# Kernel optimization log

Hardware: AMD Instinct MI355X
Metric: run time of the kernel (lower is better)

Reference implementation:

```python
import jax, jax.numpy as jnp
import numpy as np

B, T, C, H = 4, 2048, 2048, 16
DH = C // H  # 128

def setup_inputs() -> dict:
    key = jax.random.key(0)
    ks = jax.random.split(key, 5)
    s_in = 1.0 / np.sqrt(C)
    return {
        "x": jax.random.normal(ks[0], (B, T, C), dtype=jnp.float32),
        "qkv_w": jax.random.uniform(ks[1], (3 * C, C), jnp.float32, -s_in, s_in),
        "qkv_b": jax.random.uniform(ks[2], (3 * C,), jnp.float32, -s_in, s_in),
        "proj_w": jax.random.uniform(ks[3], (C, C), jnp.float32, -s_in, s_in),
        "proj_b": jax.random.uniform(ks[4], (C,), jnp.float32, -s_in, s_in),
    }

def reference(x, qkv_w, qkv_b, proj_w, proj_b):
    b, t, _ = x.shape
    qkv = x @ qkv_w.T + qkv_b                     # [B,T,3C]
    q, k, v = jnp.split(qkv, 3, axis=-1)
    # [B,T,C] -> [B,H,T,Dh]
    q = q.reshape(b, t, H, DH).transpose(0, 2, 1, 3)
    k = k.reshape(b, t, H, DH).transpose(0, 2, 1, 3)
    v = v.reshape(b, t, H, DH).transpose(0, 2, 1, 3)
    scores = jnp.einsum('bhqd,bhkd->bhqk', q, k) / jnp.sqrt(jnp.float32(DH))
    causal = jnp.tril(jnp.ones((t, t), dtype=bool))  # [T,T]
    scores = jnp.where(causal[None, None], scores, jnp.finfo(scores.dtype).min)
    att = jax.nn.softmax(scores, axis=-1)
    out = jnp.einsum('bhqk,bhkd->bhqd', att, v)   # [B,H,T,Dh]
    out = out.transpose(0, 2, 1, 3).reshape(b, t, C)
    return out @ proj_w.T + proj_b
```

## Files before the change

kernel.cpp:

```cpp
#include <hip/hip_runtime.h>
#include <stdint.h>


typedef __attribute__((ext_vector_type(8))) short bf8_t;
typedef __attribute__((ext_vector_type(4))) float f4_t;

__device__ __forceinline__ short f2bf(float f) {
  union { float f; uint32_t u; } x; x.f = f;
  uint32_t r = x.u + 0x7fffu + ((x.u >> 16) & 1u);
  return (short)(r >> 16);
}

#define GLD16(gp, lp) __builtin_amdgcn_global_load_lds( \
    (const __attribute__((address_space(1))) void*)(gp), \
    (__attribute__((address_space(3))) void*)(lp), 16, 0, 0)

#define QSCALE (0.08838834764831845f * 1.4426950408889634f)

__global__ __launch_bounds__(256) void cast3_f32_bf16(
    const float* __restrict__ a, const float* __restrict__ b,
    const float* __restrict__ c, short* __restrict__ oa,
    short* __restrict__ ob, short* __restrict__ oc,
    int na4, int nb4, int nc4) {
  int i = blockIdx.x * blockDim.x + threadIdx.x;
  const float* src; short* dst; int idx;
  if (i < na4) { src = a; dst = oa; idx = i; }
  else if (i < na4 + nb4) { src = b; dst = ob; idx = i - na4; }
  else if (i < na4 + nb4 + nc4) { src = c; dst = oc; idx = i - na4 - nb4; }
  else return;
  float4 v = ((const float4*)src)[idx];
  short4 o;
  o.x = f2bf(v.x); o.y = f2bf(v.y); o.z = f2bf(v.z); o.w = f2bf(v.w);
  ((short4*)dst)[idx] = o;
}

template <int MODE>
__global__ __launch_bounds__(256) void gemm_bt(
    const short* __restrict__ A, const short* __restrict__ Bw,
    const float* __restrict__ bias, float* __restrict__ Cout,
    short* __restrict__ Qo, short* __restrict__ Ko, short* __restrict__ Vo,
    int M, int N, int K) {
  __shared__ __attribute__((aligned(16))) short lA[8192];
  __shared__ __attribute__((aligned(16))) short lB[8192];
  const int tid = threadIdx.x;
  const int lane = tid & 63, wave = tid >> 6;
  const int quad = lane >> 4, l16 = lane & 15;
  const int wm = wave >> 1, wn = wave & 1;
  const int m0 = blockIdx.y * 128, n0 = blockIdx.x * 128;
  const int which = (MODE == 0) ? (n0 >> 11) : -1;
  const bool swapAB = (MODE == 0) && (which == 2);

  f4_t acc[4][4];
  if (!swapAB) {
#pragma unroll
    for (int j = 0; j < 4; ++j) {
      const float b0 = bias[n0 + wn * 64 + j * 16 + l16];
      const f4_t bv = {b0, b0, b0, b0};
#pragma unroll
      for (int i = 0; i < 4; ++i) acc[i][j] = bv;
    }
  } else {
#pragma unroll
    for (int i = 0; i < 4; ++i)
#pragma unroll
      for (int r = 0; r < 4; ++r) {
        const float b0 = bias[n0 + wn * 64 + i * 16 + quad * 4 + r];
#pragma unroll
        for (int j = 0; j < 4; ++j) acc[i][j][r] = b0;
      }
  }

  const char* baseA = (const char*)(A + (size_t)m0 * K);
  const char* baseB = (const char*)(Bw + (size_t)n0 * K);
  uint32_t voff[4];
#pragma unroll
  for (int r = 0; r < 4; ++r) {
    const int off = tid * 16 + r * 4096;
    const int kk = off >> 13;
    const int row = (off >> 6) & 127;
    const int col = kk * 32 + ((off & 63) >> 1);
    voff[r] = (uint32_t)(row * K + col) * 2u;
  }

  for (int k0 = 0; k0 < K; k0 += 64) {
    __syncthreads();
#pragma unroll
    for (int r = 0; r < 4; ++r) {
      const int off = tid * 16 + r * 4096;
      GLD16(baseA + voff[r], (char*)lA + off);
      GLD16(baseB + voff[r], (char*)lB + off);
    }
    baseA += 128;
    baseB += 128;
    __syncthreads();
#pragma unroll
    for (int kk = 0; kk < 2; ++kk) {
      bf8_t af[4], bfr[4];
#pragma unroll
      for (int i = 0; i < 4; ++i) {
        af[i]  = *(const bf8_t*)(lA + kk * 4096 + (wm * 64 + i * 16 + l16) * 32 + quad * 8);
        bfr[i] = *(const bf8_t*)(lB + kk * 4096 + (wn * 64 + i * 16 + l16) * 32 + quad * 8);
      }
      if (!swapAB) {
#pragma unroll
        for (int i = 0; i < 4; ++i)
#pragma unroll
          for (int j = 0; j < 4; ++j)
            acc[i][j] = __builtin_amdgcn_mfma_f32_16x16x32_bf16(af[i], bfr[j], acc[i][j], 0, 0, 0);
      } else {
#pragma unroll
        for (int i = 0; i < 4; ++i)
#pragma unroll
          for (int j = 0; j < 4; ++j)
            acc[i][j] = __builtin_amdgcn_mfma_f32_16x16x32_bf16(bfr[i], af[j], acc[i][j], 0, 0, 0);
      }
    }
  }

  if (MODE == 1) {
    const int mb = m0 + wm * 64, nb = n0 + wn * 64;
#pragma unroll
    for (int i = 0; i < 4; ++i) {
#pragma unroll
      for (int r = 0; r < 4; ++r) {
        const int m = mb + i * 16 + quad * 4 + r;
#pragma unroll
        for (int j = 0; j < 4; ++j) {
          const int n = nb + j * 16 + l16;
          Cout[(size_t)m * N + n] = acc[i][j][r];
        }
      }
    }
  } else if (!swapAB) {
    const int mb = m0 + wm * 64, nb = n0 + wn * 64;
    const int b = m0 >> 11;
    const int h = (n0 & 2047) >> 7;
    short* dst = (which == 0) ? Qo : Ko;
    const float sc = (which == 0) ? QSCALE : 1.0f;
#pragma unroll
    for (int i = 0; i < 4; ++i) {
#pragma unroll
      for (int r = 0; r < 4; ++r) {
        const int t = (mb + i * 16 + quad * 4 + r) & 2047;
#pragma unroll
        for (int j = 0; j < 4; ++j) {
          const int d = (nb + j * 16 + l16) & 127;
          dst[((size_t)((b * 16 + h) * 2048 + t)) * 128 + d] =
              f2bf(acc[i][j][r] * sc);
        }
      }
    }
  } else {
    const int b = m0 >> 11;
    const int h = (n0 & 2047) >> 7;
#pragma unroll
    for (int i = 0; i < 4; ++i) {
#pragma unroll
      for (int r = 0; r < 4; ++r) {
        const int doff = wn * 64 + i * 16 + quad * 4 + r;
#pragma unroll
        for (int j = 0; j < 4; ++j) {
          const int t = (m0 & 2047) + wm * 64 + j * 16 + l16;
          Vo[((size_t)((b * 16 + h) * 128 + doff)) * 2048 + t] =
              f2bf(acc[i][j][r]);
        }
      }
    }
  }
}

__global__ __launch_bounds__(256) void attn_fwd(
    const short* __restrict__ Qg, const short* __restrict__ Kg,
    const short* __restrict__ Vtg, short* __restrict__ Og) {
  __shared__ __attribute__((aligned(16))) short lK[64 * 128];
  __shared__ __attribute__((aligned(16))) short lV[128 * 64];
  __shared__ __attribute__((aligned(16))) short lP[4 * 2048];
  const int tid = threadIdx.x;
  const int lane = tid & 63, wave = tid >> 6;
  const int quad = lane >> 4, l16 = lane & 15;
  const int p = blockIdx.x & 7, bh = blockIdx.x >> 3;
  const size_t baseK = (size_t)bh * (2048 * 128);
  const size_t baseV = (size_t)bh * (128 * 2048);
  const int x7 = l16 & 7;
  const int b = bh >> 4, h = bh & 15;
  short* lPw = lP + wave * 2048;
  const f4_t fz = {0.f, 0.f, 0.f, 0.f};

  uint32_t vK[4], vV[4];
#pragma unroll
  for (int r = 0; r < 4; ++r) {
    const int off = tid * 16 + r * 4096;
    const int rowK = off >> 8;
    const int lcK = ((off >> 4) & 15) ^ (rowK & 7);
    vK[r] = (uint32_t)(rowK * 128 + lcK * 8) * 2u;
    const int dV = off >> 7;
    const int lcV = ((off >> 4) & 7) ^ (dV & 7);
    vV[r] = (uint32_t)(dV * 2048 + lcV * 8) * 2u;
  }

  for (int job = 0; job < 2; ++job) {
    const int bx = job ? (15 - p) : p;
    const int q0 = bx * 128;
    const int qw = q0 + wave * 32;

    bf8_t qf[2][4];
#pragma unroll
    for (int m = 0; m < 2; ++m)
#pragma unroll
      for (int dc = 0; dc < 4; ++dc)
        qf[m][dc] = *(const bf8_t*)(Qg + baseK + (size_t)(qw + m * 16 + l16) * 128 + dc * 32 + quad * 8);

    f4_t o[2][8];
#pragma unroll
    for (int m = 0; m < 2; ++m)
#pragma unroll
      for (int n = 0; n < 8; ++n) o[m][n] = fz;
    float lsum[2][4];
#pragma unroll
    for (int m = 0; m < 2; ++m)
#pragma unroll
      for (int r = 0; r < 4; ++r) lsum[m][r] = 0.f;

    const char* kbase = (const char*)(Kg + baseK);
    const char* vbase = (const char*)(Vtg + baseV);
    const int ktmax = 2 * bx + 1;
    for (int kt = 0; kt <= ktmax; ++kt) {
      const int k0 = kt * 64;
      __syncthreads();
#pragma unroll
      for (int r = 0; r < 4; ++r) {
        const int off = tid * 16 + r * 4096;
        GLD16(kbase + vK[r], (char*)lK + off);
        GLD16(vbase + vV[r], (char*)lV + off);
      }
      kbase += 16384;
      vbase += 128;
      __syncthreads();
      if (k0 >= qw + 32) continue;

      f4_t s[2][4];
#pragma unroll
      for (int m = 0; m < 2; ++m)
#pragma unroll
        for (int g = 0; g < 4; ++g) s[m][g] = fz;
#pragma unroll
      for (int g = 0; g < 4; ++g)
#pragma unroll
        for (int dc = 0; dc < 4; ++dc) {
          bf8_t kf = *(const bf8_t*)(lK + (g * 16 + l16) * 128 + (((dc * 4 + quad) ^ x7) << 3));
          s[0][g] = __builtin_amdgcn_mfma_f32_16x16x32_bf16(qf[0][dc], kf, s[0][g], 0, 0, 0);
          s[1][g] = __builtin_amdgcn_mfma_f32_16x16x32_bf16(qf[1][dc], kf, s[1][g], 0, 0, 0);
        }
#pragma unroll
      for (int m = 0; m < 2; ++m) {
        const int qbase = qw + m * 16;
        const bool nomask = (k0 + 63 <= qbase);
#pragma unroll
        for (int g = 0; g < 4; ++g) {
          const int key = k0 + g * 16 + l16;
#pragma unroll
          for (int r = 0; r < 4; ++r) {
            float pv = exp2f(s[m][g][r]);
            if (!nomask && key > qbase + quad * 4 + r) pv = 0.f;
            lsum[m][r] += pv;
            const int row = quad * 4 + r;
            lPw[m * 1024 + row * 64 + (((g * 2 + (l16 >> 3)) ^ (row & 7)) << 3) + x7] = f2bf(pv);
          }
        }
      }
      bf8_t pa[2][2];
#pragma unroll
      for (int m = 0; m < 2; ++m)
#pragma unroll
        for (int kc = 0; kc < 2; ++kc)
          pa[m][kc] = *(const bf8_t*)(lPw + m * 1024 + l16 * 64 + (((kc * 4 + quad) ^ x7) << 3));
#pragma unroll
      for (int n = 0; n < 8; ++n)
#pragma unroll
        for (int kc = 0; kc < 2; ++kc) {
          bf8_t vf = *(const bf8_t*)(lV + (n * 16 + l16) * 64 + (((kc * 4 + quad) ^ x7) << 3));
          o[0][n] = __builtin_amdgcn_mfma_f32_16x16x32_bf16(pa[0][kc], vf, o[0][n], 0, 0, 0);
          o[1][n] = __builtin_amdgcn_mfma_f32_16x16x32_bf16(pa[1][kc], vf, o[1][n], 0, 0, 0);
        }
    }
#pragma unroll
    for (int m = 0; m < 2; ++m)
#pragma unroll
      for (int r = 0; r < 4; ++r) {
        float v = lsum[m][r];
        v += __shfl_xor(v, 1, 64);
        v += __shfl_xor(v, 2, 64);
        v += __shfl_xor(v, 4, 64);
        v += __shfl_xor(v, 8, 64);
        const float inv = 1.f / v;
        const int t = qw + m * 16 + quad * 4 + r;
        const size_t orow = ((size_t)(b * 2048 + t)) * 2048 + h * 128;
#pragma unroll
        for (int n = 0; n < 8; ++n)
          Og[orow + n * 16 + l16] = f2bf(o[m][n][r] * inv);
      }
  }
}

extern "C" void kernel_launch(void* const* d_in, const int* in_sizes, int n_in,
                              void* d_out, int out_size, void* d_ws, size_t ws_size,
                              hipStream_t stream) {
  const float* x      = (const float*)d_in[0];
  const float* qkv_w  = (const float*)d_in[1];
  const float* qkv_b  = (const float*)d_in[2];
  const float* proj_w = (const float*)d_in[3];
  const float* proj_b = (const float*)d_in[4];
  float* out = (float*)d_out;

  char* ws = (char*)d_ws;
  short* xb    = (short*)(ws);
  short* wqkv  = (short*)(ws + 33554432);
  short* wproj = (short*)(ws + 58720256);
  short* qb    = (short*)(ws + 67108864);
  short* kb    = (short*)(ws + 100663296);
  short* vb    = (short*)(ws + 134217728);
  short* attb  = (short*)(ws + 167772160);

  cast3_f32_bf16<<<32768, 256, 0, stream>>>(x, qkv_w, proj_w, xb, wqkv, wproj,
                                            4194304, 3145728, 1048576);

  gemm_bt<0><<<dim3(48, 64), 256, 0, stream>>>(xb, wqkv, qkv_b, nullptr,
                                               qb, kb, vb, 8192, 6144, 2048);
  attn_fwd<<<512, 256, 0, stream>>>(qb, kb, vb, attb);
  gemm_bt<1><<<dim3(16, 64), 256, 0, stream>>>(attb, wproj, proj_b, out,
                                               nullptr, nullptr, nullptr, 8192, 2048, 2048);
}
```

Baseline: 619.5 us.

## Rewrite projection GEMMs as 256x256 double-buffered, swizzled, ping-pong scheduled kernels

Both GEMMs move from 128x128 tiles with 4 waves to 256x256 tiles with 8 waves, 128 KB of LDS and double buffering. Global-to-LDS loads for the next K steps are issued between MFMA quadrants, with barriers and s_setprio to interleave memory and compute. LDS rows are XOR-swizzled to avoid bank conflicts, and block IDs are remapped across 8 groups for cache locality. The cost is a much larger LDS footprint per block and more complex epilogue indexing. The grid shrinks to 768 and 256 blocks, which may leave some CUs idle.

Result: faster. 558.0 us (-9.9%).

```diff
diff --git a/kernel.cpp b/kernel.cpp
--- a/kernel.cpp
+++ b/kernel.cpp
@@ -34,134 +34,203 @@
   ((short4*)dst)[idx] = o;
 }
 
+
+#define BARR() do { __builtin_amdgcn_s_barrier(); \
+                    __builtin_amdgcn_sched_barrier(0); } while (0)
+#define PR1 __builtin_amdgcn_s_setprio(1)
+#define PR0 __builtin_amdgcn_s_setprio(0)
+
+#define STAGE(g, loff) do { \
+    GLD16((g) + voff0, ldsc + (loff) + dst0); \
+    GLD16((g) + voff1, ldsc + (loff) + 8192 + dst0); } while (0)
+
+#define QUAD(CI, CJ, AF, BF)                                                \
+  if (!swapAB) {                                                            \
+    _Pragma("unroll") for (int kk = 0; kk < 2; ++kk)                        \
+    _Pragma("unroll") for (int i = 0; i < 4; ++i)                           \
+    _Pragma("unroll") for (int j = 0; j < 2; ++j)                           \
+      acc[(CI) + i][(CJ) + j] = __builtin_amdgcn_mfma_f32_16x16x32_bf16(    \
+          AF[i][kk], BF[j][kk], acc[(CI) + i][(CJ) + j], 0, 0, 0);          \
+  } else {                                                                  \
+    _Pragma("unroll") for (int kk = 0; kk < 2; ++kk)                        \
+    _Pragma("unroll") for (int i = 0; i < 4; ++i)                           \
+    _Pragma("unroll") for (int j = 0; j < 2; ++j)                           \
+      acc[(CI) + i][(CJ) + j] = __builtin_amdgcn_mfma_f32_16x16x32_bf16(    \
+          BF[j][kk], AF[i][kk], acc[(CI) + i][(CJ) + j], 0, 0, 0);          \
+  }
+
 template <int MODE>
-__global__ __launch_bounds__(256) void gemm_bt(
+__global__ __launch_bounds__(512, 2) void gemm_bt(
     const short* __restrict__ A, const short* __restrict__ Bw,
     const float* __restrict__ bias, float* __restrict__ Cout,
     short* __restrict__ Qo, short* __restrict__ Ko, short* __restrict__ Vo,
     int M, int N, int K) {
-  __shared__ __attribute__((aligned(16))) short lA[8192];
-  __shared__ __attribute__((aligned(16))) short lB[8192];
+  __shared__ __attribute__((aligned(16))) char lds[131072];
   const int tid = threadIdx.x;
   const int lane = tid & 63, wave = tid >> 6;
   const int quad = lane >> 4, l16 = lane & 15;
-  const int wm = wave >> 1, wn = wave & 1;
-  const int m0 = blockIdx.y * 128, n0 = blockIdx.x * 128;
+  const int wm = wave >> 2, wn = wave & 3;
+
+  const int nwg = gridDim.x;
+  const int cpx = nwg >> 3;
+  const int bid = blockIdx.x;
+  const int swz = (bid & 7) * cpx + (bid >> 3);
+  const int nbx = N >> 8;
+  const int bm = swz / nbx, bn = swz - bm * nbx;
+  const int m0 = bm << 8, n0 = bn << 8;
+
   const int which = (MODE == 0) ? (n0 >> 11) : -1;
   const bool swapAB = (MODE == 0) && (which == 2);
 
-  f4_t acc[4][4];
+
+  f4_t acc[8][4];
   if (!swapAB) {
 #pragma unroll
     for (int j = 0; j < 4; ++j) {
-      const float b0 = bias[n0 + wn * 64 + j * 16 + l16];
+      const float b0 = bias[n0 + (j >> 1) * 128 + wn * 32 + (j & 1) * 16 + l16];
       const f4_t bv = {b0, b0, b0, b0};
 #pragma unroll
-      for (int i = 0; i < 4; ++i) acc[i][j] = bv;
+      for (int i = 0; i < 8; ++i) acc[i][j] = bv;
     }
   } else {
 #pragma unroll
-    for (int i = 0; i < 4; ++i)
+    for (int j = 0; j < 4; ++j)
 #pragma unroll
       for (int r = 0; r < 4; ++r) {
-        const float b0 = bias[n0 + wn * 64 + i * 16 + quad * 4 + r];
-#pragma unroll
-        for (int j = 0; j < 4; ++j) acc[i][j][r] = b0;
+        const float b0 =
+            bias[n0 + (j >> 1) * 128 + wn * 32 + (j & 1) * 16 + quad * 4 + r];
+#pragma unroll
+        for (int i = 0; i < 8; ++i) acc[i][j][r] = b0;
       }
   }
 
   const char* baseA = (const char*)(A + (size_t)m0 * K);
   const char* baseB = (const char*)(Bw + (size_t)n0 * K);
-  uint32_t voff[4];
-#pragma unroll
-  for (int r = 0; r < 4; ++r) {
-    const int off = tid * 16 + r * 4096;
-    const int kk = off >> 13;
-    const int row = (off >> 6) & 127;
-    const int col = kk * 32 + ((off & 63) >> 1);
-    voff[r] = (uint32_t)(row * K + col) * 2u;
-  }
-
-  for (int k0 = 0; k0 < K; k0 += 64) {
-    __syncthreads();
-#pragma unroll
-    for (int r = 0; r < 4; ++r) {
-      const int off = tid * 16 + r * 4096;
-      GLD16(baseA + voff[r], (char*)lA + off);
-      GLD16(baseB + voff[r], (char*)lB + off);
-    }
-    baseA += 128;
-    baseB += 128;
-    __syncthreads();
-#pragma unroll
-    for (int kk = 0; kk < 2; ++kk) {
-      bf8_t af[4], bfr[4];
-#pragma unroll
-      for (int i = 0; i < 4; ++i) {
-        af[i]  = *(const bf8_t*)(lA + kk * 4096 + (wm * 64 + i * 16 + l16) * 32 + quad * 8);
-        bfr[i] = *(const bf8_t*)(lB + kk * 4096 + (wn * 64 + i * 16 + l16) * 32 + quad * 8);
-      }
-      if (!swapAB) {
-#pragma unroll
-        for (int i = 0; i < 4; ++i)
-#pragma unroll
-          for (int j = 0; j < 4; ++j)
-            acc[i][j] = __builtin_amdgcn_mfma_f32_16x16x32_bf16(af[i], bfr[j], acc[i][j], 0, 0, 0);
-      } else {
-#pragma unroll
-        for (int i = 0; i < 4; ++i)
-#pragma unroll
-          for (int j = 0; j < 4; ++j)
-            acc[i][j] = __builtin_amdgcn_mfma_f32_16x16x32_bf16(bfr[i], af[j], acc[i][j], 0, 0, 0);
-      }
-    }
+  const size_t hK = (size_t)K << 8;
+  const int r0 = tid >> 3;
+  const int lg = (tid & 7) ^ (r0 & 7);
+  const uint32_t voff0 = (uint32_t)(r0 * K + lg * 8) * 2u;
+  const uint32_t voff1 = voff0 + ((uint32_t)K << 7);
+  char* ldsc = (char*)lds;
+  const int dst0 = tid * 16;
+
+  const int x7 = l16 & 7;
+  const int gx0 = (quad ^ x7) << 4;
+  const int gx1 = ((quad | 4) ^ x7) << 4;
+
+  asm volatile("s_waitcnt vmcnt(0)" ::: "memory");
+  __builtin_amdgcn_sched_barrier(0);
+
+  STAGE(baseA, 0);
+  STAGE(baseB + hK, 49152);
+  STAGE(baseA + hK, 16384);
+  STAGE(baseB, 32768);
+  STAGE(baseA + 128, 65536 + 0);
+  STAGE(baseB + hK + 128, 65536 + 49152);
+  STAGE(baseA + hK + 128, 65536 + 16384);
+  asm volatile("s_waitcnt vmcnt(6)" ::: "memory");
+  __builtin_amdgcn_sched_barrier(0);
+  __builtin_amdgcn_s_barrier();
+
+  const int NT = K >> 6;
+  bf8_t af[4][2], b0f[2][2], b1f[2][2];
+  for (int t = 0; t < NT; ++t) {
+    const int s = (t & 1) << 16;
+    const int o = s ^ 65536;
+    const size_t c1 = (size_t)(t + 1 < NT ? t + 1 : NT - 1) << 7;
+    const size_t c2 = (size_t)(t + 2 < NT ? t + 2 : NT - 1) << 7;
+    const char* pA = ldsc + s + wm * 8192 + l16 * 128;
+    const char* pB = ldsc + s + 32768 + wn * 4096 + l16 * 128;
+
+#pragma unroll
+    for (int i = 0; i < 4; ++i) {
+      af[i][0] = *(const bf8_t*)(pA + i * 2048 + gx0);
+      af[i][1] = *(const bf8_t*)(pA + i * 2048 + gx1);
+    }
+#pragma unroll
+    for (int j = 0; j < 2; ++j) {
+      b0f[j][0] = *(const bf8_t*)(pB + j * 2048 + gx0);
+      b0f[j][1] = *(const bf8_t*)(pB + j * 2048 + gx1);
+    }
+    STAGE(baseB + c1, o + 32768);
+    BARR();
+    PR1; QUAD(0, 0, af, b0f); PR0;
+    BARR();
+
+#pragma unroll
+    for (int j = 0; j < 2; ++j) {
+      b1f[j][0] = *(const bf8_t*)(pB + 16384 + j * 2048 + gx0);
+      b1f[j][1] = *(const bf8_t*)(pB + 16384 + j * 2048 + gx1);
+    }
+    STAGE(baseA + c2, s + 0);
+    BARR();
+    PR1; QUAD(0, 2, af, b1f); PR0;
+    BARR();
+
+#pragma unroll
+    for (int i = 0; i < 4; ++i) {
+      af[i][0] = *(const bf8_t*)(pA + 16384 + i * 2048 + gx0);
+      af[i][1] = *(const bf8_t*)(pA + 16384 + i * 2048 + gx1);
+    }
+    STAGE(baseB + hK + c2, s + 49152);
+    BARR();
+    PR1; QUAD(4, 2, af, b1f); PR0;
+    BARR();
+
+    STAGE(baseA + hK + c2, s + 16384);
+    BARR();
+    PR1; QUAD(4, 0, af, b0f); PR0;
+    asm volatile("s_waitcnt vmcnt(6)" ::: "memory");
+    __builtin_amdgcn_sched_barrier(0);
+    __builtin_amdgcn_s_barrier();
   }
 
   if (MODE == 1) {
-    const int mb = m0 + wm * 64, nb = n0 + wn * 64;
-#pragma unroll
-    for (int i = 0; i < 4; ++i) {
+#pragma unroll
+    for (int i = 0; i < 8; ++i) {
+      const int mg = m0 + (i >> 2) * 128 + wm * 64 + (i & 3) * 16 + quad * 4;
 #pragma unroll
       for (int r = 0; r < 4; ++r) {
-        const int m = mb + i * 16 + quad * 4 + r;
+        const size_t mrow = (size_t)(mg + r) * N;
 #pragma unroll
         for (int j = 0; j < 4; ++j) {
-          const int n = nb + j * 16 + l16;
-          Cout[(size_t)m * N + n] = acc[i][j][r];
+          const int ng = n0 + (j >> 1) * 128 + wn * 32 + (j & 1) * 16 + l16;
+          Cout[mrow + ng] = acc[i][j][r];
         }
       }
     }
   } else if (!swapAB) {
-    const int mb = m0 + wm * 64, nb = n0 + wn * 64;
-    const int b = m0 >> 11;
-    const int h = (n0 & 2047) >> 7;
     short* dst = (which == 0) ? Qo : Ko;
     const float sc = (which == 0) ? QSCALE : 1.0f;
 #pragma unroll
-    for (int i = 0; i < 4; ++i) {
+    for (int i = 0; i < 8; ++i) {
+      const int mg = m0 + (i >> 2) * 128 + wm * 64 + (i & 3) * 16 + quad * 4;
 #pragma unroll
       for (int r = 0; r < 4; ++r) {
-        const int t = (mb + i * 16 + quad * 4 + r) & 2047;
+        const int m = mg + r;
+        const int b = m >> 11, tt = m & 2047;
 #pragma unroll
         for (int j = 0; j < 4; ++j) {
-          const int d = (nb + j * 16 + l16) & 127;
-          dst[((size_t)((b * 16 + h) * 2048 + t)) * 128 + d] =
+          const int ng = n0 + (j >> 1) * 128 + wn * 32 + (j & 1) * 16 + l16;
+          const int h = (ng & 2047) >> 7, d = ng & 127;
+          dst[((size_t)((b * 16 + h) * 2048 + tt)) * 128 + d] =
               f2bf(acc[i][j][r] * sc);
         }
       }
     }
   } else {
-    const int b = m0 >> 11;
-    const int h = (n0 & 2047) >> 7;
-#pragma unroll
-    for (int i = 0; i < 4; ++i) {
-#pragma unroll
-      for (int r = 0; r < 4; ++r) {
-        const int doff = wn * 64 + i * 16 + quad * 4 + r;
-#pragma unroll
-        for (int j = 0; j < 4; ++j) {
-          const int t = (m0 & 2047) + wm * 64 + j * 16 + l16;
-          Vo[((size_t)((b * 16 + h) * 128 + doff)) * 2048 + t] =
+#pragma unroll
+    for (int i = 0; i < 8; ++i) {
+      const int mg = m0 + (i >> 2) * 128 + wm * 64 + (i & 3) * 16 + l16;
+      const int b = mg >> 11, tt = mg & 2047;
+#pragma unroll
+      for (int j = 0; j < 4; ++j) {
+        const int nb = n0 + (j >> 1) * 128 + wn * 32 + (j & 1) * 16 + quad * 4;
+#pragma unroll
+        for (int r = 0; r < 4; ++r) {
+          const int ng = nb + r;
+          const int h = (ng & 2047) >> 7, d = ng & 127;
+          Vo[((size_t)((b * 16 + h) * 128 + d)) * 2048 + tt] =
               f2bf(acc[i][j][r]);
         }
       }
@@ -324,9 +393,9 @@
   cast3_f32_bf16<<<32768, 256, 0, stream>>>(x, qkv_w, proj_w, xb, wqkv, wproj,
                                             4194304, 3145728, 1048576);
 
-  gemm_bt<0><<<dim3(48, 64), 256, 0, stream>>>(xb, wqkv, qkv_b, nullptr,
-                                               qb, kb, vb, 8192, 6144, 2048);
+  gemm_bt<0><<<768, 512, 0, stream>>>(xb, wqkv, qkv_b, nullptr,
+                                      qb, kb, vb, 8192, 6144, 2048);
   attn_fwd<<<512, 256, 0, stream>>>(qb, kb, vb, attb);
-  gemm_bt<1><<<dim3(16, 64), 256, 0, stream>>>(attb, wproj, proj_b, out,
-                                               nullptr, nullptr, nullptr, 8192, 2048, 2048);
+  gemm_bt<1><<<256, 512, 0, stream>>>(attb, wproj, proj_b, out,
+                                      nullptr, nullptr, nullptr, 8192, 2048, 2048);
 }
```
